# Performance work log

Hardware: AMD Instinct MI355X
Metric: run time of the kernel (lower is better)

## Reference

```python
import jax, jax.numpy as jnp
import numpy as np

B, N_IN, N_H, N_OUT = 128, 256, 256, 256


def _bimul(W, X):
    # MatrixBiMul: bilinear map W X W^T, W: [out, in], X: [b, in, in] -> [b, out, out]
    return jnp.einsum('oi,bij,qj->boq', W, X, W)


def setup_inputs() -> dict:
    key = jax.random.key(0)
    ks = jax.random.split(key, 12)
    s_in = 1.0 / np.sqrt(N_IN)
    s_h = 1.0 / np.sqrt(N_H)
    return {
        'input': jax.random.normal(ks[0], (B, N_IN, N_IN), jnp.float32),
        'hidden': jax.random.normal(ks[1], (B, N_H, N_H), jnp.float32),
        'cell': jax.random.normal(ks[2], (B, N_H, N_H), jnp.float32),
        'W_fx': jax.random.normal(ks[3], (N_H, N_IN), jnp.float32) * s_in,
        'W_ix': jax.random.normal(ks[4], (N_H, N_IN), jnp.float32) * s_in,
        'W_ox': jax.random.normal(ks[5], (N_OUT, N_IN), jnp.float32) * s_in,
        'W_gx': jax.random.normal(ks[6], (N_H, N_IN), jnp.float32) * s_in,
        'W_fh': jax.random.normal(ks[7], (N_H, N_H), jnp.float32) * s_h,
        'W_ih': jax.random.normal(ks[8], (N_H, N_H), jnp.float32) * s_h,
        'W_oh': jax.random.normal(ks[9], (N_OUT, N_H), jnp.float32) * s_h,
        'W_gh': jax.random.normal(ks[10], (N_H, N_H), jnp.float32) * s_h,
        'W_oc': jax.random.normal(ks[11], (N_OUT, N_H), jnp.float32) * s_h,
    }


def reference(input, hidden, cell, W_fx, W_ix, W_ox, W_gx, W_fh, W_ih, W_oh, W_gh, W_oc):
    fgate = jax.nn.relu(_bimul(W_fx, input) + _bimul(W_fh, hidden))
    igate = jax.nn.relu(_bimul(W_ix, input) + _bimul(W_ih, hidden))
    ogate = jax.nn.relu(_bimul(W_ox, input) + _bimul(W_oh, hidden))
    ggate = jax.nn.relu(_bimul(W_gx, input) + _bimul(W_gh, hidden))
    c = fgate + cell + igate + ggate  # note: additive, as in source (not fgate*cell)
    h = ogate + jax.nn.relu(_bimul(W_oc, c))
    return (h, c)
```

## Files before the change

### kernel.cpp

```cpp
#include <hip/hip_runtime.h>

typedef __bf16 bf16x8 __attribute__((ext_vector_type(8)));
typedef float f32x4 __attribute__((ext_vector_type(4)));

__device__ __forceinline__ unsigned short f2bf(float f) {
    unsigned int u = __builtin_bit_cast(unsigned int, f);
    u += 0x7fff + ((u >> 16) & 1);
    return (unsigned short)(u >> 16);
}

__device__ __forceinline__ void stage_pair(
    const unsigned short* __restrict__ Ap, int lda,
    const unsigned short* __restrict__ Bp, int ldb,
    unsigned short* lds, int k0, int tid)
{
#pragma unroll
    for (int it = 0; it < 4; ++it) {
        int li = it * 256 + tid;
        int row = li >> 3;
        int sc = ((li & 7) ^ (row & 7)) * 8;
        __builtin_amdgcn_global_load_lds(
            (const __attribute__((address_space(1))) void*)(Ap + (long)row * lda + k0 + sc),
            (__attribute__((address_space(3))) void*)&lds[li * 8], 16, 0, 0);
        __builtin_amdgcn_global_load_lds(
            (const __attribute__((address_space(1))) void*)(Bp + (long)row * ldb + k0 + sc),
            (__attribute__((address_space(3))) void*)&lds[8192 + li * 8], 16, 0, 0);
    }
}

__device__ __forceinline__ void compute_tile(
    const unsigned short* lds, int lane, int wm, int wn, f32x4 (&acc)[4][4])
{
#pragma unroll
    for (int kk = 0; kk < 2; ++kk) {
        const int cl = kk * 4 + (lane >> 4);
        bf16x8 af[4], bfr[4];
#pragma unroll
        for (int m = 0; m < 4; ++m) {
            int row = wm + m * 16 + (lane & 15);
            af[m] = *(const bf16x8*)&lds[row * 64 + ((cl ^ (row & 7)) * 8)];
        }
#pragma unroll
        for (int n = 0; n < 4; ++n) {
            int row = wn + n * 16 + (lane & 15);
            bfr[n] = *(const bf16x8*)&lds[8192 + row * 64 + ((cl ^ (row & 7)) * 8)];
        }
#pragma unroll
        for (int m = 0; m < 4; ++m)
#pragma unroll
            for (int n = 0; n < 4; ++n)
                acc[m][n] = __builtin_amdgcn_mfma_f32_16x16x32_bf16(af[m], bfr[n], acc[m][n], 0, 0, 0);
    }
}

__global__ __launch_bounds__(256)
void cvt_xh(const float* __restrict__ X, const float* __restrict__ H,
            unsigned short* __restrict__ XHb)
{
    long e = (long)(blockIdx.x * 256 + threadIdx.x) * 8;
    const float* s = (e < 8388608) ? (X + e) : (H + (e - 8388608));
    float4 a = *(const float4*)s;
    float4 c = *(const float4*)(s + 4);
    uint4 uv;
    uv.x = (unsigned)f2bf(a.x) | ((unsigned)f2bf(a.y) << 16);
    uv.y = (unsigned)f2bf(a.z) | ((unsigned)f2bf(a.w) << 16);
    uv.z = (unsigned)f2bf(c.x) | ((unsigned)f2bf(c.y) << 16);
    uv.w = (unsigned)f2bf(c.z) | ((unsigned)f2bf(c.w) << 16);
    *(uint4*)&XHb[e] = uv;
}

__global__ __launch_bounds__(256)
void cvt_weights(const float* __restrict__ fx, const float* __restrict__ ix,
                 const float* __restrict__ ox, const float* __restrict__ gx,
                 const float* __restrict__ fh, const float* __restrict__ ih,
                 const float* __restrict__ oh, const float* __restrict__ gh,
                 const float* __restrict__ oc,
                 unsigned short* __restrict__ Wcat, unsigned short* __restrict__ Wocb)
{
    int idx = blockIdx.x * 256 + threadIdx.x;
    if (idx < 524288) {
        int g = idx >> 17;
        int rem = idx & 131071;
        int q = rem >> 9;
        int j = rem & 511;
        const float* xs = (g == 0) ? fx : (g == 1) ? ix : (g == 2) ? ox : gx;
        const float* hs = (g == 0) ? fh : (g == 1) ? ih : (g == 2) ? oh : gh;
        float v = (j < 256) ? xs[q * 256 + j] : hs[q * 256 + (j - 256)];
        Wcat[idx] = f2bf(v);
    } else if (idx < 589824) {
        int k = idx - 524288;
        Wocb[k] = f2bf(oc[k]);
    }
}

__global__ __launch_bounds__(256)
void gemm_s1(const unsigned short* __restrict__ Wcat,
             const unsigned short* __restrict__ XHb,
             unsigned short* __restrict__ Tcat)
{
    __shared__ alignas(16) unsigned short lds[16384];

    const int tid = threadIdx.x;
    const int lane = tid & 63;
    const int w = tid >> 6;

    int d = blockIdx.x + 4 * blockIdx.y + 512 * blockIdx.z;
    int swz = (d & 7) * 512 + (d >> 3);
    const int x = swz & 3;
    const int b = (swz >> 2) & 127;
    const int gz = swz >> 9;
    const int g = gz >> 1, hf = gz & 1;
    const int tq = (x >> 1) * 128;
    const int ti = (x & 1) * 128;
    const int wm = (w >> 1) * 64;
    const int wn = (w & 1) * 64;

    const unsigned short* Ap = Wcat + (long)g * 131072 + (long)tq * 512 + hf * 256;
    const unsigned short* Bp = XHb + (long)hf * 8388608 + (long)b * 65536 + (long)ti * 256;

    f32x4 acc[4][4];
#pragma unroll
    for (int m = 0; m < 4; ++m)
#pragma unroll
        for (int n = 0; n < 4; ++n)
            acc[m][n] = (f32x4){0.f, 0.f, 0.f, 0.f};

#pragma unroll
    for (int t = 0; t < 4; ++t) {
        if (t > 0) __syncthreads();
        stage_pair(Ap, 512, Bp, 256, lds, t * 64, tid);
        __syncthreads();
        compute_tile(lds, lane, wm, wn, acc);
    }

    unsigned short* Cb = Tcat + (long)g * 16777216 + (long)b * 131072 + hf * 256;
    const int r0 = (lane >> 4) * 4;
    const int c0 = lane & 15;
#pragma unroll
    for (int m = 0; m < 4; ++m)
#pragma unroll
        for (int n = 0; n < 4; ++n)
#pragma unroll
            for (int r = 0; r < 4; ++r) {
                int row = tq + wm + m * 16 + r0 + r;
                int col = ti + wn + n * 16 + c0;
                Cb[(long)row * 512 + col] = f2bf(acc[m][n][r]);
            }
}

__global__ __launch_bounds__(256)
void gemm_gateB(const unsigned short* __restrict__ Tcat,
                const unsigned short* __restrict__ Wcat,
                const float* __restrict__ cell,
                float* __restrict__ out_c, float* __restrict__ out_h,
                unsigned short* __restrict__ cb16)
{
    __shared__ alignas(16) unsigned short lds[32768];

    const int tid = threadIdx.x;
    const int lane = tid & 63;
    const int w = tid >> 6;

    int orig = blockIdx.x + 4 * blockIdx.y;
    int swz = (orig & 7) * 64 + (orig >> 3);
    const int x = swz & 3;
    const int b = swz >> 2;
    const int to = (x >> 1) * 128;
    const int tq = (x & 1) * 128;
    const int wm = (w >> 1) * 64;
    const int wn = (w & 1) * 64;

    f32x4 accc[4][4], acc[4][4];
#pragma unroll
    for (int m = 0; m < 4; ++m)
#pragma unroll
        for (int n = 0; n < 4; ++n) {
            accc[m][n] = (f32x4){0.f, 0.f, 0.f, 0.f};
            acc[m][n] = (f32x4){0.f, 0.f, 0.f, 0.f};
        }

    {
        const unsigned short* Ap0 = Wcat + (long)to * 512;
        const unsigned short* Bp0 = Tcat + (long)b * 131072 + (long)tq * 512;
        stage_pair(Ap0, 512, Bp0, 512, lds, 0, tid);
    }
    for (int u = 0; u < 32; ++u) {
        __syncthreads();
        if (u + 1 < 32) {
            int s = (u + 1) >> 3;
            int gv = s ^ (s >> 1);
            const unsigned short* Ap = Wcat + (long)gv * 131072 + (long)to * 512;
            const unsigned short* Bp = Tcat + (long)gv * 16777216 + (long)b * 131072 + (long)tq * 512;
            stage_pair(Ap, 512, Bp, 512, lds + ((u + 1) & 1) * 16384, ((u + 1) & 7) * 64, tid);
        }
        compute_tile(lds + (u & 1) * 16384, lane, wm, wn, acc);
        if ((u & 7) == 7 && u != 31) {
#pragma unroll
            for (int m = 0; m < 4; ++m)
#pragma unroll
                for (int n = 0; n < 4; ++n)
#pragma unroll
                    for (int r = 0; r < 4; ++r) {
                        float v = acc[m][n][r];
                        accc[m][n][r] += (v > 0.f ? v : 0.f);
                        acc[m][n][r] = 0.f;
                    }
        }
    }

    const float* cb = cell + (long)b * 65536;
    float* co = out_c + (long)b * 65536;
    float* ho = out_h + (long)b * 65536;
    unsigned short* cbo = cb16 + (long)b * 65536;
    const int r0 = (lane >> 4) * 4;
    const int c0 = lane & 15;
#pragma unroll
    for (int m = 0; m < 4; ++m)
#pragma unroll
        for (int n = 0; n < 4; ++n)
#pragma unroll
            for (int r = 0; r < 4; ++r) {
                int row = to + wm + m * 16 + r0 + r;
                int col = tq + wn + n * 16 + c0;
                long idx = (long)row * 256 + col;
                float cv = accc[m][n][r] + cb[idx];
                co[idx] = cv;
                cbo[idx] = f2bf(cv);
                float v = acc[m][n][r];
                ho[idx] = (v > 0.f ? v : 0.f);
            }
}

template <int MODE>
__global__ __launch_bounds__(256)
void gemm_nt2(const unsigned short* __restrict__ A, int lda, long sAy,
              const unsigned short* __restrict__ B, int ldb, long sBy,
              void* __restrict__ Cv, int ldc, long sCy)
{
    __shared__ alignas(16) unsigned short lds[32768];

    const int tid = threadIdx.x;
    const int lane = tid & 63;
    const int w = tid >> 6;

    int orig = blockIdx.x + 4 * blockIdx.y;
    int swz = (orig & 7) * 64 + (orig >> 3);
    const int x = swz & 3;
    const int b = swz >> 2;
    const int tm = (x >> 1) * 128;
    const int tn = (x & 1) * 128;
    const int wm = (w >> 1) * 64;
    const int wn = (w & 1) * 64;

    const unsigned short* Ap = A + b * sAy + (long)tm * lda;
    const unsigned short* Bp = B + b * sBy + (long)tn * ldb;

    f32x4 acc[4][4];
#pragma unroll
    for (int m = 0; m < 4; ++m)
#pragma unroll
        for (int n = 0; n < 4; ++n)
            acc[m][n] = (f32x4){0.f, 0.f, 0.f, 0.f};

    stage_pair(Ap, lda, Bp, ldb, lds, 0, tid);
#pragma unroll
    for (int t = 0; t < 4; ++t) {
        __syncthreads();
        if (t + 1 < 4)
            stage_pair(Ap, lda, Bp, ldb, lds + ((t + 1) & 1) * 16384, (t + 1) * 64, tid);
        compute_tile(lds + (t & 1) * 16384, lane, wm, wn, acc);
    }

    const long coff = b * sCy;
    const int r0 = (lane >> 4) * 4;
    const int c0 = lane & 15;

    if (MODE == 0) {
        unsigned short* C = (unsigned short*)Cv + coff;
#pragma unroll
        for (int m = 0; m < 4; ++m)
#pragma unroll
            for (int n = 0; n < 4; ++n)
#pragma unroll
                for (int r = 0; r < 4; ++r) {
                    int row = tm + wm + m * 16 + r0 + r;
                    int col = tn + wn + n * 16 + c0;
                    C[(long)row * ldc + col] = f2bf(acc[m][n][r]);
                }
    } else {
        float* C = (float*)Cv + coff;
#pragma unroll
        for (int m = 0; m < 4; ++m)
#pragma unroll
            for (int n = 0; n < 4; ++n)
#pragma unroll
                for (int r = 0; r < 4; ++r) {
                    int row = tm + wm + m * 16 + r0 + r;
                    int col = tn + wn + n * 16 + c0;
                    long idx = (long)row * ldc + col;
                    float v = acc[m][n][r];
                    C[idx] += (v > 0.f ? v : 0.f);
                }
    }
}

extern "C" void kernel_launch(void* const* d_in, const int* in_sizes, int n_in,
                              void* d_out, int out_size, void* d_ws, size_t ws_size,
                              hipStream_t stream)
{
    (void)in_sizes; (void)n_in; (void)out_size; (void)ws_size;

    const float* X    = (const float*)d_in[0];
    const float* H    = (const float*)d_in[1];
    const float* cell = (const float*)d_in[2];
    const float* Wxp[4] = {(const float*)d_in[3], (const float*)d_in[4],
                           (const float*)d_in[5], (const float*)d_in[6]};
    const float* Whp[4] = {(const float*)d_in[7], (const float*)d_in[8],
                           (const float*)d_in[9], (const float*)d_in[10]};
    const float* Wocf = (const float*)d_in[11];

    float* out_h = (float*)d_out;
    float* out_c = out_h + 8388608;

    unsigned short* ws   = (unsigned short*)d_ws;
    unsigned short* XHb  = ws;
    unsigned short* Wcat = ws + 16777216;
    unsigned short* Wocb = ws + 17301504;
    unsigned short* Tcat = ws + 17367040;
    unsigned short* cb16 = ws + 84475904;
    unsigned short* ScT  = ws + 92864512;

    cvt_xh<<<dim3(8192), 256, 0, stream>>>(X, H, XHb);
    cvt_weights<<<dim3(2304), 256, 0, stream>>>(Wxp[0], Wxp[1], Wxp[2], Wxp[3],
                                                Whp[0], Whp[1], Whp[2], Whp[3],
                                                Wocf, Wcat, Wocb);
    gemm_s1<<<dim3(4, 128, 8), 256, 0, stream>>>(Wcat, XHb, Tcat);
    gemm_gateB<<<dim3(4, 128), 256, 0, stream>>>(Tcat, Wcat, cell, out_c, out_h, cb16);
    gemm_nt2<0><<<dim3(4, 128), 256, 0, stream>>>(
        Wocb, 256, 0L, cb16, 256, 65536L,
        (void*)ScT, 256, 65536L);
    gemm_nt2<2><<<dim3(4, 128), 256, 0, stream>>>(
        Wocb, 256, 0L, ScT, 256, 65536L,
        (void*)out_h, 256, 65536L);
}
```

Before: 193.4 us.

## Load weight A-fragments directly from global, stage only B through LDS

The weight operand (shared across the batch and likely cache-resident) is now read straight from global memory into registers, in the MFMA fragment layout. Only the activation operand is staged in LDS, which halves LDS use per block and may raise occupancy. gemm_s1 also gains double buffering instead of its serial stage-sync-compute loop. The risk is that uncoalesced, strided 16-byte global reads of A on every k-step may stall the MFMA pipeline more than the LDS staging they replace.

```diff
diff --git a/kernel.cpp b/kernel.cpp
--- a/kernel.cpp
+++ b/kernel.cpp
@@ -9,8 +9,7 @@
     return (unsigned short)(u >> 16);
 }
 
-__device__ __forceinline__ void stage_pair(
-    const unsigned short* __restrict__ Ap, int lda,
+__device__ __forceinline__ void stage_B(
     const unsigned short* __restrict__ Bp, int ldb,
     unsigned short* lds, int k0, int tid)
 {
@@ -20,37 +19,39 @@
         int row = li >> 3;
         int sc = ((li & 7) ^ (row & 7)) * 8;
         __builtin_amdgcn_global_load_lds(
-            (const __attribute__((address_space(1))) void*)(Ap + (long)row * lda + k0 + sc),
+            (const __attribute__((address_space(1))) void*)(Bp + (long)row * ldb + k0 + sc),
             (__attribute__((address_space(3))) void*)&lds[li * 8], 16, 0, 0);
-        __builtin_amdgcn_global_load_lds(
-            (const __attribute__((address_space(1))) void*)(Bp + (long)row * ldb + k0 + sc),
-            (__attribute__((address_space(3))) void*)&lds[8192 + li * 8], 16, 0, 0);
-    }
-}
-
-__device__ __forceinline__ void compute_tile(
-    const unsigned short* lds, int lane, int wm, int wn, f32x4 (&acc)[4][4])
-{
+    }
+}
+
+__device__ __forceinline__ void compute_ag(
+    const unsigned short* __restrict__ Ag, int lda, int k0,
+    const unsigned short* ldsB, int lane, int wm, int wn, f32x4 (&acc)[4][4])
+{
+    bf16x8 af[2][4], bfr[2][4];
 #pragma unroll
     for (int kk = 0; kk < 2; ++kk) {
         const int cl = kk * 4 + (lane >> 4);
-        bf16x8 af[4], bfr[4];
-#pragma unroll
-        for (int m = 0; m < 4; ++m) {
-            int row = wm + m * 16 + (lane & 15);
-            af[m] = *(const bf16x8*)&lds[row * 64 + ((cl ^ (row & 7)) * 8)];
-        }
+#pragma unroll
+        for (int m = 0; m < 4; ++m)
+            af[kk][m] = *(const bf16x8*)&Ag[(long)(wm + m * 16 + (lane & 15)) * lda + k0 + cl * 8];
+    }
+#pragma unroll
+    for (int kk = 0; kk < 2; ++kk) {
+        const int cl = kk * 4 + (lane >> 4);
 #pragma unroll
         for (int n = 0; n < 4; ++n) {
             int row = wn + n * 16 + (lane & 15);
-            bfr[n] = *(const bf16x8*)&lds[8192 + row * 64 + ((cl ^ (row & 7)) * 8)];
+            bfr[kk][n] = *(const bf16x8*)&ldsB[row * 64 + ((cl ^ (row & 7)) * 8)];
         }
+    }
+#pragma unroll
+    for (int kk = 0; kk < 2; ++kk)
 #pragma unroll
         for (int m = 0; m < 4; ++m)
 #pragma unroll
             for (int n = 0; n < 4; ++n)
-                acc[m][n] = __builtin_amdgcn_mfma_f32_16x16x32_bf16(af[m], bfr[n], acc[m][n], 0, 0, 0);
-    }
+                acc[m][n] = __builtin_amdgcn_mfma_f32_16x16x32_bf16(af[kk][m], bfr[kk][n], acc[m][n], 0, 0, 0);
 }
 
 __global__ __launch_bounds__(256)
@@ -115,7 +116,7 @@
     const int wm = (w >> 1) * 64;
     const int wn = (w & 1) * 64;
 
-    const unsigned short* Ap = Wcat + (long)g * 131072 + (long)tq * 512 + hf * 256;
+    const unsigned short* Ag = Wcat + (long)g * 131072 + (long)tq * 512 + hf * 256;
     const unsigned short* Bp = XHb + (long)hf * 8388608 + (long)b * 65536 + (long)ti * 256;
 
     f32x4 acc[4][4];
@@ -125,12 +126,13 @@
         for (int n = 0; n < 4; ++n)
             acc[m][n] = (f32x4){0.f, 0.f, 0.f, 0.f};
 
+    stage_B(Bp, 256, lds, 0, tid);
 #pragma unroll
     for (int t = 0; t < 4; ++t) {
-        if (t > 0) __syncthreads();
-        stage_pair(Ap, 512, Bp, 256, lds, t * 64, tid);
         __syncthreads();
-        compute_tile(lds, lane, wm, wn, acc);
+        if (t + 1 < 4)
+            stage_B(Bp, 256, lds + ((t + 1) & 1) * 8192, (t + 1) * 64, tid);
+        compute_ag(Ag, 512, t * 64, lds + (t & 1) * 8192, lane, wm, wn, acc);
     }
 
     unsigned short* Cb = Tcat + (long)g * 16777216 + (long)b * 131072 + hf * 256;
@@ -155,7 +157,7 @@
                 float* __restrict__ out_c, float* __restrict__ out_h,
                 unsigned short* __restrict__ cb16)
 {
-    __shared__ alignas(16) unsigned short lds[32768];
+    __shared__ alignas(16) unsigned short lds[16384];
 
     const int tid = threadIdx.x;
     const int lane = tid & 63;
@@ -179,21 +181,19 @@
             acc[m][n] = (f32x4){0.f, 0.f, 0.f, 0.f};
         }
 
-    {
-        const unsigned short* Ap0 = Wcat + (long)to * 512;
-        const unsigned short* Bp0 = Tcat + (long)b * 131072 + (long)tq * 512;
-        stage_pair(Ap0, 512, Bp0, 512, lds, 0, tid);
-    }
+    stage_B(Tcat + (long)b * 131072 + (long)tq * 512, 512, lds, 0, tid);
     for (int u = 0; u < 32; ++u) {
         __syncthreads();
         if (u + 1 < 32) {
-            int s = (u + 1) >> 3;
-            int gv = s ^ (s >> 1);
-            const unsigned short* Ap = Wcat + (long)gv * 131072 + (long)to * 512;
-            const unsigned short* Bp = Tcat + (long)gv * 16777216 + (long)b * 131072 + (long)tq * 512;
-            stage_pair(Ap, 512, Bp, 512, lds + ((u + 1) & 1) * 16384, ((u + 1) & 7) * 64, tid);
+            int s2 = (u + 1) >> 3;
+            int gv2 = s2 ^ (s2 >> 1);
+            const unsigned short* Bp = Tcat + (long)gv2 * 16777216 + (long)b * 131072 + (long)tq * 512;
+            stage_B(Bp, 512, lds + ((u + 1) & 1) * 8192, ((u + 1) & 7) * 64, tid);
         }
-        compute_tile(lds + (u & 1) * 16384, lane, wm, wn, acc);
+        int s = u >> 3;
+        int gv = s ^ (s >> 1);
+        const unsigned short* Ag = Wcat + (long)gv * 131072 + (long)to * 512;
+        compute_ag(Ag, 512, (u & 7) * 64, lds + (u & 1) * 8192, lane, wm, wn, acc);
         if ((u & 7) == 7 && u != 31) {
 #pragma unroll
             for (int m = 0; m < 4; ++m)
@@ -233,11 +233,11 @@
 
 template <int MODE>
 __global__ __launch_bounds__(256)
-void gemm_nt2(const unsigned short* __restrict__ A, int lda, long sAy,
+void gemm_nt2(const unsigned short* __restrict__ A, int lda,
               const unsigned short* __restrict__ B, int ldb, long sBy,
               void* __restrict__ Cv, int ldc, long sCy)
 {
-    __shared__ alignas(16) unsigned short lds[32768];
+    __shared__ alignas(16) unsigned short lds[16384];
 
     const int tid = threadIdx.x;
     const int lane = tid & 63;
@@ -252,7 +252,7 @@
     const int wm = (w >> 1) * 64;
     const int wn = (w & 1) * 64;
 
-    const unsigned short* Ap = A + b * sAy + (long)tm * lda;
+    const unsigned short* Ag = A + (long)tm * lda;
     const unsigned short* Bp = B + b * sBy + (long)tn * ldb;
 
     f32x4 acc[4][4];
@@ -262,13 +262,13 @@
         for (int n = 0; n < 4; ++n)
             acc[m][n] = (f32x4){0.f, 0.f, 0.f, 0.f};
 
-    stage_pair(Ap, lda, Bp, ldb, lds, 0, tid);
+    stage_B(Bp, ldb, lds, 0, tid);
 #pragma unroll
     for (int t = 0; t < 4; ++t) {
         __syncthreads();
         if (t + 1 < 4)
-            stage_pair(Ap, lda, Bp, ldb, lds + ((t + 1) & 1) * 16384, (t + 1) * 64, tid);
-        compute_tile(lds + (t & 1) * 16384, lane, wm, wn, acc);
+            stage_B(Bp, ldb, lds + ((t + 1) & 1) * 8192, (t + 1) * 64, tid);
+        compute_ag(Ag, lda, t * 64, lds + (t & 1) * 8192, lane, wm, wn, acc);
     }
 
     const long coff = b * sCy;
@@ -337,9 +337,9 @@
     gemm_s1<<<dim3(4, 128, 8), 256, 0, stream>>>(Wcat, XHb, Tcat);
     gemm_gateB<<<dim3(4, 128), 256, 0, stream>>>(Tcat, Wcat, cell, out_c, out_h, cb16);
     gemm_nt2<0><<<dim3(4, 128), 256, 0, stream>>>(
-        Wocb, 256, 0L, cb16, 256, 65536L,
+        Wocb, 256, cb16, 256, 65536L,
         (void*)ScT, 256, 65536L);
     gemm_nt2<2><<<dim3(4, 128), 256, 0, stream>>>(
-        Wocb, 256, 0L, ScT, 256, 65536L,
+        Wocb, 256, ScT, 256, 65536L,
         (void*)out_h, 256, 65536L);
 }
```

Result: slower. 290.7 us (+50.3%).

## Switch GEMMs to BK=32 triple-buffered LDS pipeline with partial vmcnt waits

Applied to the files above, without the earlier changes.

All three GEMM kernels change from 64-wide K stages with double (or single) buffering to 32-wide K stages held in a three-slot LDS ring. Loads are issued two stages ahead, and each stage waits with a partial vmcnt before the barrier, so one stage's loads stay in flight during compute. The LDS swizzle is changed to match the 32-element rows, and gemm_s1 also gains prefetching it lacked. The cost is twice as many barriers per K, and correctness now depends on the manual waitcnt counts matching the number of outstanding loads.

```diff
diff --git a/kernel.cpp b/kernel.cpp
--- a/kernel.cpp
+++ b/kernel.cpp
@@ -9,48 +9,62 @@
     return (unsigned short)(u >> 16);
 }
 
-__device__ __forceinline__ void stage_pair(
+__device__ __forceinline__ int swz32(int ck, int row) {
+    return ((ck ^ ((row >> 1) & 3)) * 8);
+}
+
+__device__ __forceinline__ void stage32(
     const unsigned short* __restrict__ Ap, int lda,
     const unsigned short* __restrict__ Bp, int ldb,
-    unsigned short* lds, int k0, int tid)
-{
-#pragma unroll
-    for (int it = 0; it < 4; ++it) {
+    unsigned short* buf, int k0, int tid)
+{
+#pragma unroll
+    for (int it = 0; it < 2; ++it) {
         int li = it * 256 + tid;
-        int row = li >> 3;
-        int sc = ((li & 7) ^ (row & 7)) * 8;
+        int row = li >> 2;
+        int sc = swz32(li & 3, row);
         __builtin_amdgcn_global_load_lds(
             (const __attribute__((address_space(1))) void*)(Ap + (long)row * lda + k0 + sc),
-            (__attribute__((address_space(3))) void*)&lds[li * 8], 16, 0, 0);
+            (__attribute__((address_space(3))) void*)&buf[li * 8], 16, 0, 0);
         __builtin_amdgcn_global_load_lds(
             (const __attribute__((address_space(1))) void*)(Bp + (long)row * ldb + k0 + sc),
-            (__attribute__((address_space(3))) void*)&lds[8192 + li * 8], 16, 0, 0);
-    }
-}
-
-__device__ __forceinline__ void compute_tile(
-    const unsigned short* lds, int lane, int wm, int wn, f32x4 (&acc)[4][4])
-{
-#pragma unroll
-    for (int kk = 0; kk < 2; ++kk) {
-        const int cl = kk * 4 + (lane >> 4);
-        bf16x8 af[4], bfr[4];
-#pragma unroll
-        for (int m = 0; m < 4; ++m) {
-            int row = wm + m * 16 + (lane & 15);
-            af[m] = *(const bf16x8*)&lds[row * 64 + ((cl ^ (row & 7)) * 8)];
-        }
-#pragma unroll
-        for (int n = 0; n < 4; ++n) {
-            int row = wn + n * 16 + (lane & 15);
-            bfr[n] = *(const bf16x8*)&lds[8192 + row * 64 + ((cl ^ (row & 7)) * 8)];
-        }
-#pragma unroll
-        for (int m = 0; m < 4; ++m)
-#pragma unroll
-            for (int n = 0; n < 4; ++n)
-                acc[m][n] = __builtin_amdgcn_mfma_f32_16x16x32_bf16(af[m], bfr[n], acc[m][n], 0, 0, 0);
-    }
+            (__attribute__((address_space(3))) void*)&buf[4096 + li * 8], 16, 0, 0);
+    }
+}
+
+__device__ __forceinline__ void compute32(
+    const unsigned short* buf, int lane, int wm, int wn, f32x4 (&acc)[4][4])
+{
+    const int cl = lane >> 4;
+    bf16x8 af[4], bfr[4];
+#pragma unroll
+    for (int m = 0; m < 4; ++m) {
+        int row = wm + m * 16 + (lane & 15);
+        af[m] = *(const bf16x8*)&buf[row * 32 + swz32(cl, row)];
+    }
+#pragma unroll
+    for (int n = 0; n < 4; ++n) {
+        int row = wn + n * 16 + (lane & 15);
+        bfr[n] = *(const bf16x8*)&buf[4096 + row * 32 + swz32(cl, row)];
+    }
+#pragma unroll
+    for (int m = 0; m < 4; ++m)
+#pragma unroll
+        for (int n = 0; n < 4; ++n)
+            acc[m][n] = __builtin_amdgcn_mfma_f32_16x16x32_bf16(af[m], bfr[n], acc[m][n], 0, 0, 0);
+}
+
+__device__ __forceinline__ void wait_bar4() {
+    asm volatile("s_waitcnt vmcnt(4)" ::: "memory");
+    __builtin_amdgcn_sched_barrier(0);
+    __builtin_amdgcn_s_barrier();
+    __builtin_amdgcn_sched_barrier(0);
+}
+__device__ __forceinline__ void wait_bar0() {
+    asm volatile("s_waitcnt vmcnt(0)" ::: "memory");
+    __builtin_amdgcn_sched_barrier(0);
+    __builtin_amdgcn_s_barrier();
+    __builtin_amdgcn_sched_barrier(0);
 }
 
 __global__ __launch_bounds__(256)
@@ -98,7 +112,7 @@
              const unsigned short* __restrict__ XHb,
              unsigned short* __restrict__ Tcat)
 {
-    __shared__ alignas(16) unsigned short lds[16384];
+    __shared__ alignas(16) unsigned short lds[24576];
 
     const int tid = threadIdx.x;
     const int lane = tid & 63;
@@ -125,12 +139,14 @@
         for (int n = 0; n < 4; ++n)
             acc[m][n] = (f32x4){0.f, 0.f, 0.f, 0.f};
 
-#pragma unroll
-    for (int t = 0; t < 4; ++t) {
-        if (t > 0) __syncthreads();
-        stage_pair(Ap, 512, Bp, 256, lds, t * 64, tid);
-        __syncthreads();
-        compute_tile(lds, lane, wm, wn, acc);
+    stage32(Ap, 512, Bp, 256, lds, 0, tid);
+    stage32(Ap, 512, Bp, 256, lds + 8192, 32, tid);
+#pragma unroll
+    for (int t = 0; t < 8; ++t) {
+        if (t < 7) wait_bar4(); else wait_bar0();
+        if (t + 2 < 8)
+            stage32(Ap, 512, Bp, 256, lds + ((t + 2) % 3) * 8192, (t + 2) * 32, tid);
+        compute32(lds + (t % 3) * 8192, lane, wm, wn, acc);
     }
 
     unsigned short* Cb = Tcat + (long)g * 16777216 + (long)b * 131072 + hf * 256;
@@ -155,7 +171,7 @@
                 float* __restrict__ out_c, float* __restrict__ out_h,
                 unsigned short* __restrict__ cb16)
 {
-    __shared__ alignas(16) unsigned short lds[32768];
+    __shared__ alignas(16) unsigned short lds[24576];
 
     const int tid = threadIdx.x;
     const int lane = tid & 63;
@@ -179,22 +195,22 @@
             acc[m][n] = (f32x4){0.f, 0.f, 0.f, 0.f};
         }
 
-    {
-        const unsigned short* Ap0 = Wcat + (long)to * 512;
-        const unsigned short* Bp0 = Tcat + (long)b * 131072 + (long)tq * 512;
-        stage_pair(Ap0, 512, Bp0, 512, lds, 0, tid);
-    }
-    for (int u = 0; u < 32; ++u) {
-        __syncthreads();
-        if (u + 1 < 32) {
-            int s = (u + 1) >> 3;
-            int gv = s ^ (s >> 1);
-            const unsigned short* Ap = Wcat + (long)gv * 131072 + (long)to * 512;
-            const unsigned short* Bp = Tcat + (long)gv * 16777216 + (long)b * 131072 + (long)tq * 512;
-            stage_pair(Ap, 512, Bp, 512, lds + ((u + 1) & 1) * 16384, ((u + 1) & 7) * 64, tid);
+    const unsigned short* Ab = Wcat + (long)to * 512;
+    const unsigned short* Bb = Tcat + (long)b * 131072 + (long)tq * 512;
+
+    stage32(Ab, 512, Bb, 512, lds, 0, tid);
+    stage32(Ab, 512, Bb, 512, lds + 8192, 32, tid);
+    for (int u = 0; u < 64; ++u) {
+        if (u < 63) wait_bar4(); else wait_bar0();
+        if (u + 2 < 64) {
+            int s2 = (u + 2) >> 4;
+            int gv2 = s2 ^ (s2 >> 1);
+            stage32(Ab + (long)gv2 * 131072, 512,
+                    Bb + (long)gv2 * 16777216, 512,
+                    lds + ((u + 2) % 3) * 8192, ((u + 2) & 15) * 32, tid);
         }
-        compute_tile(lds + (u & 1) * 16384, lane, wm, wn, acc);
-        if ((u & 7) == 7 && u != 31) {
+        compute32(lds + (u % 3) * 8192, lane, wm, wn, acc);
+        if ((u & 15) == 15 && u != 63) {
 #pragma unroll
             for (int m = 0; m < 4; ++m)
 #pragma unroll
@@ -237,7 +253,7 @@
               const unsigned short* __restrict__ B, int ldb, long sBy,
               void* __restrict__ Cv, int ldc, long sCy)
 {
-    __shared__ alignas(16) unsigned short lds[32768];
+    __shared__ alignas(16) unsigned short lds[24576];
 
     const int tid = threadIdx.x;
     const int lane = tid & 63;
@@ -262,13 +278,14 @@
         for (int n = 0; n < 4; ++n)
             acc[m][n] = (f32x4){0.f, 0.f, 0.f, 0.f};
 
-    stage_pair(Ap, lda, Bp, ldb, lds, 0, tid);
-#pragma unroll
-    for (int t = 0; t < 4; ++t) {
-        __syncthreads();
-        if (t + 1 < 4)
-            stage_pair(Ap, lda, Bp, ldb, lds + ((t + 1) & 1) * 16384, (t + 1) * 64, tid);
-        compute_tile(lds + (t & 1) * 16384, lane, wm, wn, acc);
+    stage32(Ap, lda, Bp, ldb, lds, 0, tid);
+    stage32(Ap, lda, Bp, ldb, lds + 8192, 32, tid);
+#pragma unroll
+    for (int t = 0; t < 8; ++t) {
+        if (t < 7) wait_bar4(); else wait_bar0();
+        if (t + 2 < 8)
+            stage32(Ap, lda, Bp, ldb, lds + ((t + 2) % 3) * 8192, (t + 2) * 32, tid);
+        compute32(lds + (t % 3) * 8192, lane, wm, wn, acc);
     }
 
     const long coff = b * sCy;
```

Measured after the change: 210.5 us. 1.09x slower.

## Fuse both W_oc bilinear GEMMs into one kernel with LDS-resident intermediate

Applied to the files above, without the earlier changes.

Merges the two W_oc GEMM launches into one kernel. Each block computes a 256x128 slice of the intermediate W_oc·c^T product and keeps it in swizzled LDS, then runs the second GEMM from LDS, so the ScT round trip through global memory disappears. The two conversion kernels are also merged into a single launch. In exchange the grid shrinks to 256 blocks, each using 128KB of LDS, and every block recomputes its first-stage product for only half the output columns. That lowers occupancy and parallelism.

```diff
diff --git a/kernel.cpp b/kernel.cpp
--- a/kernel.cpp
+++ b/kernel.cpp
@@ -28,6 +28,21 @@
     }
 }
 
+__device__ __forceinline__ void stage_one(
+    const unsigned short* __restrict__ Ap, int lda,
+    unsigned short* buf, int k0, int tid)
+{
+#pragma unroll
+    for (int it = 0; it < 4; ++it) {
+        int li = it * 256 + tid;
+        int row = li >> 3;
+        int sc = ((li & 7) ^ (row & 7)) * 8;
+        __builtin_amdgcn_global_load_lds(
+            (const __attribute__((address_space(1))) void*)(Ap + (long)row * lda + k0 + sc),
+            (__attribute__((address_space(3))) void*)&buf[li * 8], 16, 0, 0);
+    }
+}
+
 __device__ __forceinline__ void compute_tile(
     const unsigned short* lds, int lane, int wm, int wn, f32x4 (&acc)[4][4])
 {
@@ -53,43 +68,69 @@
     }
 }
 
+__device__ __forceinline__ void compute_bsc(
+    const unsigned short* bufA, const unsigned short* Sc, int k0,
+    int lane, int wm, int wn, f32x4 (&acc)[4][4])
+{
+#pragma unroll
+    for (int kk = 0; kk < 2; ++kk) {
+        const int cl = kk * 4 + (lane >> 4);
+        bf16x8 af[4], bfr[4];
+#pragma unroll
+        for (int m = 0; m < 4; ++m) {
+            int row = wm + m * 16 + (lane & 15);
+            af[m] = *(const bf16x8*)&bufA[row * 64 + ((cl ^ (row & 7)) * 8)];
+        }
+#pragma unroll
+        for (int n = 0; n < 4; ++n) {
+            int row = wn + n * 16 + (lane & 15);
+            bfr[n] = *(const bf16x8*)&Sc[row * 256 + k0 + ((cl ^ (row & 7)) * 8)];
+        }
+#pragma unroll
+        for (int m = 0; m < 4; ++m)
+#pragma unroll
+            for (int n = 0; n < 4; ++n)
+                acc[m][n] = __builtin_amdgcn_mfma_f32_16x16x32_bf16(af[m], bfr[n], acc[m][n], 0, 0, 0);
+    }
+}
+
 __global__ __launch_bounds__(256)
-void cvt_xh(const float* __restrict__ X, const float* __restrict__ H,
-            unsigned short* __restrict__ XHb)
-{
-    long e = (long)(blockIdx.x * 256 + threadIdx.x) * 8;
-    const float* s = (e < 8388608) ? (X + e) : (H + (e - 8388608));
-    float4 a = *(const float4*)s;
-    float4 c = *(const float4*)(s + 4);
-    uint4 uv;
-    uv.x = (unsigned)f2bf(a.x) | ((unsigned)f2bf(a.y) << 16);
-    uv.y = (unsigned)f2bf(a.z) | ((unsigned)f2bf(a.w) << 16);
-    uv.z = (unsigned)f2bf(c.x) | ((unsigned)f2bf(c.y) << 16);
-    uv.w = (unsigned)f2bf(c.z) | ((unsigned)f2bf(c.w) << 16);
-    *(uint4*)&XHb[e] = uv;
-}
-
-__global__ __launch_bounds__(256)
-void cvt_weights(const float* __restrict__ fx, const float* __restrict__ ix,
-                 const float* __restrict__ ox, const float* __restrict__ gx,
-                 const float* __restrict__ fh, const float* __restrict__ ih,
-                 const float* __restrict__ oh, const float* __restrict__ gh,
-                 const float* __restrict__ oc,
-                 unsigned short* __restrict__ Wcat, unsigned short* __restrict__ Wocb)
-{
-    int idx = blockIdx.x * 256 + threadIdx.x;
-    if (idx < 524288) {
-        int g = idx >> 17;
-        int rem = idx & 131071;
-        int q = rem >> 9;
-        int j = rem & 511;
-        const float* xs = (g == 0) ? fx : (g == 1) ? ix : (g == 2) ? ox : gx;
-        const float* hs = (g == 0) ? fh : (g == 1) ? ih : (g == 2) ? oh : gh;
-        float v = (j < 256) ? xs[q * 256 + j] : hs[q * 256 + (j - 256)];
-        Wcat[idx] = f2bf(v);
-    } else if (idx < 589824) {
-        int k = idx - 524288;
-        Wocb[k] = f2bf(oc[k]);
+void cvt_all(const float* __restrict__ X, const float* __restrict__ H,
+             unsigned short* __restrict__ XHb,
+             const float* __restrict__ fx, const float* __restrict__ ix,
+             const float* __restrict__ ox, const float* __restrict__ gx,
+             const float* __restrict__ fh, const float* __restrict__ ih,
+             const float* __restrict__ oh, const float* __restrict__ gh,
+             const float* __restrict__ oc,
+             unsigned short* __restrict__ Wcat, unsigned short* __restrict__ Wocb)
+{
+    int bid = blockIdx.x;
+    if (bid < 8192) {
+        long e = ((long)bid * 256 + threadIdx.x) * 8;
+        const float* s = (e < 8388608) ? (X + e) : (H + (e - 8388608));
+        float4 a = *(const float4*)s;
+        float4 c = *(const float4*)(s + 4);
+        uint4 uv;
+        uv.x = (unsigned)f2bf(a.x) | ((unsigned)f2bf(a.y) << 16);
+        uv.y = (unsigned)f2bf(a.z) | ((unsigned)f2bf(a.w) << 16);
+        uv.z = (unsigned)f2bf(c.x) | ((unsigned)f2bf(c.y) << 16);
+        uv.w = (unsigned)f2bf(c.z) | ((unsigned)f2bf(c.w) << 16);
+        *(uint4*)&XHb[e] = uv;
+    } else {
+        int idx = (bid - 8192) * 256 + threadIdx.x;
+        if (idx < 524288) {
+            int g = idx >> 17;
+            int rem = idx & 131071;
+            int q = rem >> 9;
+            int j = rem & 511;
+            const float* xs = (g == 0) ? fx : (g == 1) ? ix : (g == 2) ? ox : gx;
+            const float* hs = (g == 0) ? fh : (g == 1) ? ih : (g == 2) ? oh : gh;
+            float v = (j < 256) ? xs[q * 256 + j] : hs[q * 256 + (j - 256)];
+            Wcat[idx] = f2bf(v);
+        } else if (idx < 589824) {
+            int k = idx - 524288;
+            Wocb[k] = f2bf(oc[k]);
+        }
     }
 }
 
@@ -231,75 +272,92 @@
             }
 }
 
-template <int MODE>
 __global__ __launch_bounds__(256)
-void gemm_nt2(const unsigned short* __restrict__ A, int lda, long sAy,
-              const unsigned short* __restrict__ B, int ldb, long sBy,
-              void* __restrict__ Cv, int ldc, long sCy)
-{
-    __shared__ alignas(16) unsigned short lds[32768];
+void gemm_woc(const unsigned short* __restrict__ Wocb,
+              const unsigned short* __restrict__ cb16,
+              float* __restrict__ out_h)
+{
+    __shared__ alignas(16) unsigned short stg[32768];
+    __shared__ alignas(16) unsigned short Sc[32768];
 
     const int tid = threadIdx.x;
     const int lane = tid & 63;
     const int w = tid >> 6;
 
-    int orig = blockIdx.x + 4 * blockIdx.y;
-    int swz = (orig & 7) * 64 + (orig >> 3);
-    const int x = swz & 3;
-    const int b = swz >> 2;
-    const int tm = (x >> 1) * 128;
-    const int tn = (x & 1) * 128;
+    int orig = blockIdx.x + 2 * blockIdx.y;
+    int swz = (orig & 7) * 32 + (orig >> 3);
+    const int b = swz >> 1;
+    const int tq = (swz & 1) * 128;
     const int wm = (w >> 1) * 64;
     const int wn = (w & 1) * 64;
-
-    const unsigned short* Ap = A + b * sAy + (long)tm * lda;
-    const unsigned short* Bp = B + b * sBy + (long)tn * ldb;
-
-    f32x4 acc[4][4];
-#pragma unroll
-    for (int m = 0; m < 4; ++m)
-#pragma unroll
-        for (int n = 0; n < 4; ++n)
-            acc[m][n] = (f32x4){0.f, 0.f, 0.f, 0.f};
-
-    stage_pair(Ap, lda, Bp, ldb, lds, 0, tid);
-#pragma unroll
-    for (int t = 0; t < 4; ++t) {
-        __syncthreads();
-        if (t + 1 < 4)
-            stage_pair(Ap, lda, Bp, ldb, lds + ((t + 1) & 1) * 16384, (t + 1) * 64, tid);
-        compute_tile(lds + (t & 1) * 16384, lane, wm, wn, acc);
-    }
-
-    const long coff = b * sCy;
     const int r0 = (lane >> 4) * 4;
     const int c0 = lane & 15;
 
-    if (MODE == 0) {
-        unsigned short* C = (unsigned short*)Cv + coff;
+#pragma unroll
+    for (int t2 = 0; t2 < 2; ++t2) {
+        const unsigned short* Ap = Wocb + (long)tq * 256;
+        const unsigned short* Bp = cb16 + (long)b * 65536 + (long)(t2 * 128) * 256;
+
+        f32x4 acc[4][4];
+#pragma unroll
+        for (int m = 0; m < 4; ++m)
+#pragma unroll
+            for (int n = 0; n < 4; ++n)
+                acc[m][n] = (f32x4){0.f, 0.f, 0.f, 0.f};
+
+        stage_pair(Ap, 256, Bp, 256, stg, 0, tid);
+#pragma unroll
+        for (int t = 0; t < 4; ++t) {
+            __syncthreads();
+            if (t + 1 < 4)
+                stage_pair(Ap, 256, Bp, 256, stg + ((t + 1) & 1) * 16384, (t + 1) * 64, tid);
+            compute_tile(stg + (t & 1) * 16384, lane, wm, wn, acc);
+        }
 #pragma unroll
         for (int m = 0; m < 4; ++m)
 #pragma unroll
             for (int n = 0; n < 4; ++n)
 #pragma unroll
                 for (int r = 0; r < 4; ++r) {
-                    int row = tm + wm + m * 16 + r0 + r;
-                    int col = tn + wn + n * 16 + c0;
-                    C[(long)row * ldc + col] = f2bf(acc[m][n][r]);
+                    int qrow = wm + m * 16 + r0 + r;
+                    int icol = t2 * 128 + wn + n * 16 + c0;
+                    int addr = qrow * 256 + (icol & ~63)
+                             + ((((icol >> 3) & 7) ^ (qrow & 7)) * 8) + (icol & 7);
+                    Sc[addr] = f2bf(acc[m][n][r]);
                 }
-    } else {
-        float* C = (float*)Cv + coff;
+    }
+
+    float* ho = out_h + (long)b * 65536;
+#pragma unroll
+    for (int ot = 0; ot < 2; ++ot) {
+        const unsigned short* Ap = Wocb + (long)(ot * 128) * 256;
+
+        f32x4 acc[4][4];
+#pragma unroll
+        for (int m = 0; m < 4; ++m)
+#pragma unroll
+            for (int n = 0; n < 4; ++n)
+                acc[m][n] = (f32x4){0.f, 0.f, 0.f, 0.f};
+
+        stage_one(Ap, 256, stg, 0, tid);
+#pragma unroll
+        for (int t = 0; t < 4; ++t) {
+            __syncthreads();
+            if (t + 1 < 4)
+                stage_one(Ap, 256, stg + ((t + 1) & 1) * 16384, (t + 1) * 64, tid);
+            compute_bsc(stg + (t & 1) * 16384, Sc, t * 64, lane, wm, wn, acc);
+        }
 #pragma unroll
         for (int m = 0; m < 4; ++m)
 #pragma unroll
             for (int n = 0; n < 4; ++n)
 #pragma unroll
                 for (int r = 0; r < 4; ++r) {
-                    int row = tm + wm + m * 16 + r0 + r;
-                    int col = tn + wn + n * 16 + c0;
-                    long idx = (long)row * ldc + col;
+                    int orow = ot * 128 + wm + m * 16 + r0 + r;
+                    int qcol = tq + wn + n * 16 + c0;
+                    long idx = (long)orow * 256 + qcol;
                     float v = acc[m][n][r];
-                    C[idx] += (v > 0.f ? v : 0.f);
+                    ho[idx] += (v > 0.f ? v : 0.f);
                 }
     }
 }
@@ -328,18 +386,12 @@
     unsigned short* Wocb = ws + 17301504;
     unsigned short* Tcat = ws + 17367040;
     unsigned short* cb16 = ws + 84475904;
-    unsigned short* ScT  = ws + 92864512;
-
-    cvt_xh<<<dim3(8192), 256, 0, stream>>>(X, H, XHb);
-    cvt_weights<<<dim3(2304), 256, 0, stream>>>(Wxp[0], Wxp[1], Wxp[2], Wxp[3],
-                                                Whp[0], Whp[1], Whp[2], Whp[3],
-                                                Wocf, Wcat, Wocb);
+
+    cvt_all<<<dim3(10496), 256, 0, stream>>>(X, H, XHb,
+                                             Wxp[0], Wxp[1], Wxp[2], Wxp[3],
+                                             Whp[0], Whp[1], Whp[2], Whp[3],
+                                             Wocf, Wcat, Wocb);
     gemm_s1<<<dim3(4, 128, 8), 256, 0, stream>>>(Wcat, XHb, Tcat);
     gemm_gateB<<<dim3(4, 128), 256, 0, stream>>>(Tcat, Wcat, cell, out_c, out_h, cb16);
-    gemm_nt2<0><<<dim3(4, 128), 256, 0, stream>>>(
-        Wocb, 256, 0L, cb16, 256, 65536L,
-        (void*)ScT, 256, 65536L);
-    gemm_nt2<2><<<dim3(4, 128), 256, 0, stream>>>(
-        Wocb, 256, 0L, ScT, 256, 65536L,
-        (void*)out_h, 256, 65536L);
-}
+    gemm_woc<<<dim3(2, 128), 256, 0, stream>>>(Wocb, cb16, out_h);
+}
```

Measured after the change: 171.5 us. -11.3%, faster.
